# Kernel tuning notes

Hardware: AMD Instinct MI355X
Metric: run time of the kernel (lower is better)

## Reference

```python
import jax, jax.numpy as jnp
import numpy as np

BATCH, T, H, N = 16, 4096, 512, 512  # batch, seq_len, d_model, d_hidden
R_MAX, R_MIN, MAX_PHASE = 1.0, 0.0, 6.28


def setup_inputs() -> dict:
    key = jax.random.key(0)
    ks = jax.random.split(key, 8)
    u_k = jax.random.normal(ks[0], (BATCH, T, H), jnp.float32)
    x0_real = jnp.zeros((BATCH, N), jnp.float32)
    x0_imag = jnp.zeros((BATCH, N), jnp.float32)
    # LRU eigenvalue parameterization (Orvieto et al. 2023)
    u1 = jax.random.uniform(ks[1], (N,), jnp.float32)
    u2 = jax.random.uniform(ks[2], (N,), jnp.float32)
    nu_log = jnp.log(-0.5 * jnp.log(u1 * (R_MAX**2 - R_MIN**2) + R_MIN**2))
    theta_log = jnp.log(MAX_PHASE * u2)
    B_re = jax.random.normal(ks[3], (N, H), jnp.float32) / np.sqrt(2.0 * H)
    B_im = jax.random.normal(ks[4], (N, H), jnp.float32) / np.sqrt(2.0 * H)
    C_re = jax.random.normal(ks[5], (H, N), jnp.float32) / np.sqrt(N)
    C_im = jax.random.normal(ks[6], (H, N), jnp.float32) / np.sqrt(N)
    D = jax.random.normal(ks[7], (H,), jnp.float32)
    return dict(x0_real=x0_real, x0_imag=x0_imag, u_k=u_k, nu_log=nu_log,
                theta_log=theta_log, B_re=B_re, B_im=B_im, C_re=C_re,
                C_im=C_im, D=D)


def reference(x0_real, x0_imag, u_k, nu_log, theta_log, B_re, B_im, C_re, C_im, D):
    # diagonal complex eigenvalues lambda in the unit disk
    lam = jnp.exp(-jnp.exp(nu_log) + 1j * jnp.exp(theta_log))          # [N] complex64
    gamma = jnp.sqrt(1.0 - jnp.abs(lam) ** 2).astype(jnp.float32)       # [N]
    Bmat = (B_re + 1j * B_im) * gamma[:, None]                          # [N,H]
    # input projection: Bu[b,t,n] = sum_h Bmat[n,h] * u[b,t,h]
    Bu = jnp.einsum('bth,nh->btn', u_k.astype(jnp.complex64), Bmat)     # [B,T,N]
    # fold initial state into first step: x_1 = lam*x_0 + Bu_1
    x0 = x0_real + 1j * x0_imag                                         # [B,N]
    Bu = Bu.at[:, 0].add(lam[None, :] * x0)
    a = jnp.broadcast_to(lam, Bu.shape)                                 # [B,T,N]

    def combine(e1, e2):
        a1, b1 = e1
        a2, b2 = e2
        return a1 * a2, a2 * b1 + b2

    # parallel associative scan of x_k = lam*x_{k-1} + Bu_k
    _, xs = jax.lax.associative_scan(combine, (a, Bu), axis=1)          # [B,T,N]
    C = C_re + 1j * C_im                                                # [H,N]
    outs = jnp.einsum('btn,hn->bth', xs, C).real + D * u_k              # [B,T,H]
    return xs[:, -1], outs
```

## Files before the change

kernel.cpp:

```cpp
#include <hip/hip_runtime.h>

#define BATCH 16
#define TSEQ  4096
#define HDIM  512
#define NDIM  512
#define NCHUNK 64
#define LCHUNK 64

using f32x4  = __attribute__((ext_vector_type(4))) float;
using bf16x8 = __attribute__((ext_vector_type(8))) short;

typedef const __attribute__((address_space(1))) void GV;
typedef __attribute__((address_space(3))) void LV;

__device__ __forceinline__ void gload16(const void* g, void* l) {
  __builtin_amdgcn_global_load_lds((GV*)g, (LV*)l, 16, 0, 0);
}
__device__ __forceinline__ unsigned short f2bf(float f) {
  unsigned u = __float_as_uint(f);
  return (unsigned short)((u + 0x7fffu + ((u >> 16) & 1u)) >> 16);
}
__device__ __forceinline__ float bf2f(unsigned short s) {
  return __uint_as_float(((unsigned)s) << 16);
}

__global__ void prep_params(const float* __restrict__ nu_log,
                            const float* __restrict__ theta_log,
                            float* lam_re, float* lam_im, float* gam,
                            float* lamL_re, float* lamL_im) {
  int n = threadIdx.x;
  float en = expf(nu_log[n]);
  float th = expf(theta_log[n]);
  float r  = expf(-en);
  lam_re[n] = r * cosf(th);
  lam_im[n] = r * sinf(th);
  float r2 = expf(-2.f * en);
  gam[n] = sqrtf(fmaxf(1.f - r2, 0.f));
  float rL  = expf(-(float)LCHUNK * en);
  float thL = (float)LCHUNK * th;
  lamL_re[n] = rL * cosf(thL);
  lamL_im[n] = rL * sinf(thL);
}

__global__ void prep_bcat(const float* __restrict__ B_re, const float* __restrict__ B_im,
                          const float* __restrict__ gam, unsigned short* __restrict__ Bcat) {
  int idx = blockIdx.x * 256 + threadIdx.x;
  int h   = idx & (HDIM - 1);
  int row = idx >> 9;
  int n   = row >> 1;
  float g = gam[n];
  float v = (row & 1) ? B_im[n * HDIM + h] : B_re[n * HDIM + h];
  Bcat[idx] = f2bf(g * v);
}

__global__ void prep_ccat(const float* __restrict__ C_re, const float* __restrict__ C_im,
                          unsigned short* __restrict__ Ccat) {
  int idx = blockIdx.x * 256 + threadIdx.x;
  int col = idx & (2 * NDIM - 1);
  int h   = idx >> 10;
  int n   = col >> 1;
  float v = (col & 1) ? -C_im[h * NDIM + n] : C_re[h * NDIM + n];
  Ccat[idx] = f2bf(v);
}

__global__ void conv_u(const float4* __restrict__ u, ushort4* __restrict__ ub, int n4) {
  int idx = blockIdx.x * 256 + threadIdx.x;
  if (idx >= n4) return;
  float4 v = u[idx];
  ushort4 o;
  o.x = f2bf(v.x); o.y = f2bf(v.y); o.z = f2bf(v.z); o.w = f2bf(v.w);
  ub[idx] = o;
}

template <int K, bool OUTBF>
__global__ __launch_bounds__(256, 3)
void gemm97(const unsigned short* __restrict__ A,
            const unsigned short* __restrict__ Bm,
            void* __restrict__ Co, int Ncol, int Nd,
            const unsigned short* __restrict__ ub,
            const float* __restrict__ Dv) {
  __shared__ char lds[32768];
  const int tid  = threadIdx.x;
  const int wave = tid >> 6, lane = tid & 63;
  const int wr = (wave >> 1) * 64, wc = (wave & 1) * 64;

  int nwg = gridDim.x;
  int bid = blockIdx.x;
  int wg  = (bid & 7) * (nwg >> 3) + (bid >> 3);
  int bn = wg % Ncol, bm = wg / Ncol;
  const long rowBase = (long)bm * 128;
  const long colBase = (long)bn * 128;

  const int colE = 8 * ((tid & 7) ^ ((tid >> 3) & 7));
  const unsigned short* srcA[4];
  const unsigned short* srcB[4];
#pragma unroll
  for (int r = 0; r < 4; r++) {
    srcA[r] = A  + (rowBase + r * 32 + (tid >> 3)) * (long)K + colE;
    srcB[r] = Bm + (colBase + r * 32 + (tid >> 3)) * (long)K + colE;
  }

  f32x4 acc[4][4];
#pragma unroll
  for (int i = 0; i < 4; i++)
#pragma unroll
    for (int j = 0; j < 4; j++) acc[i][j] = (f32x4){0.f, 0.f, 0.f, 0.f};

  const int rsub = lane & 15;
  const int sx   = (lane & 7) << 4;
  const int ke   = (lane >> 4) << 4;

  for (int kt = 0; kt < K; kt += 64) {
    __syncthreads();
#pragma unroll
    for (int r = 0; r < 4; r++) {
      gload16(srcA[r] + kt, &lds[r * 4096 + tid * 16]);
      gload16(srcB[r] + kt, &lds[16384 + r * 4096 + tid * 16]);
    }
    __syncthreads();
#pragma unroll
    for (int kk = 0; kk < 64; kk += 32) {
      bf16x8 af[4], bf[4];
#pragma unroll
      for (int i = 0; i < 4; i++) {
        int off = (((wr + i * 16 + rsub) << 7) + kk * 2 + ke) ^ sx;
        af[i] = *(const bf16x8*)&lds[off];
      }
#pragma unroll
      for (int j = 0; j < 4; j++) {
        int off = 16384 + ((((wc + j * 16 + rsub) << 7) + kk * 2 + ke) ^ sx);
        bf[j] = *(const bf16x8*)&lds[off];
      }
#pragma unroll
      for (int i = 0; i < 4; i++)
#pragma unroll
        for (int j = 0; j < 4; j++)
          acc[i][j] = __builtin_amdgcn_mfma_f32_16x16x32_bf16(af[i], bf[j], acc[i][j], 0, 0, 0);
    }
  }

  const int cc = lane & 15, r4 = (lane >> 4) * 4;
#pragma unroll
  for (int i = 0; i < 4; i++) {
#pragma unroll
    for (int j = 0; j < 4; j++) {
      long col = colBase + wc + j * 16 + cc;
#pragma unroll
      for (int r = 0; r < 4; r++) {
        long row = rowBase + wr + i * 16 + r4 + r;
        if (OUTBF) {
          ((unsigned short*)Co)[row * (long)Nd + col] = f2bf(acc[i][j][r]);
        } else {
          float d = Dv[col];
          ((float*)Co)[row * (long)Nd + col] =
              acc[i][j][r] + d * bf2f(ub[row * (long)Nd + col]);
        }
      }
    }
  }
}

__global__ void scan_carry(const unsigned* __restrict__ Bu,
                           const float* __restrict__ lam_re, const float* __restrict__ lam_im,
                           float2* __restrict__ V) {
  int idx  = blockIdx.x * 256 + threadIdx.x;
  int n    = idx & (NDIM - 1);
  int c    = (idx >> 9) & (NCHUNK - 1);
  int bloc = idx >> 15;
  float lr = lam_re[n], li = lam_im[n];
  float xr = 0.f, xi = 0.f;
  long base = ((long)bloc * TSEQ + c * LCHUNK) * NDIM + n;
#pragma unroll 4
  for (int j = 0; j < LCHUNK; j++) {
    unsigned pv = Bu[base + (long)j * NDIM];
    float br = bf2f((unsigned short)(pv & 0xffff));
    float bi = bf2f((unsigned short)(pv >> 16));
    float nr = lr * xr - li * xi + br;
    float ni = lr * xi + li * xr + bi;
    xr = nr; xi = ni;
  }
  V[idx] = make_float2(xr, xi);
}

__global__ void scan_combine(const float2* __restrict__ V,
                             const float* __restrict__ lamL_re, const float* __restrict__ lamL_im,
                             const float* __restrict__ x0r, const float* __restrict__ x0i,
                             int b0, float2* __restrict__ In) {
  int idx  = blockIdx.x * 256 + threadIdx.x;
  int n    = idx & (NDIM - 1);
  int bloc = idx >> 9;
  int b    = b0 + bloc;
  float lr = lamL_re[n], li = lamL_im[n];
  float sr = x0r[b * NDIM + n], si = x0i[b * NDIM + n];
  long base = (long)bloc * NCHUNK * NDIM + n;
  for (int c = 0; c < NCHUNK; c++) {
    In[base + c * NDIM] = make_float2(sr, si);
    float2 v = V[base + c * NDIM];
    float nr = lr * sr - li * si + v.x;
    float ni = lr * si + li * sr + v.y;
    sr = nr; si = ni;
  }
}

__global__ void scan_apply(const unsigned* __restrict__ Bu, const float2* __restrict__ In,
                           const float* __restrict__ lam_re, const float* __restrict__ lam_im,
                           unsigned int* __restrict__ xsb, float* __restrict__ fs,
                           int b0, int fs_mode) {
  int idx  = blockIdx.x * 256 + threadIdx.x;
  int n    = idx & (NDIM - 1);
  int c    = (idx >> 9) & (NCHUNK - 1);
  int bloc = idx >> 15;
  float lr = lam_re[n], li = lam_im[n];
  float2 s = In[idx];
  float xr = s.x, xi = s.y;
  long base = ((long)bloc * TSEQ + c * LCHUNK) * NDIM + n;
#pragma unroll 4
  for (int j = 0; j < LCHUNK; j++) {
    unsigned pv = Bu[base + (long)j * NDIM];
    float br = bf2f((unsigned short)(pv & 0xffff));
    float bi = bf2f((unsigned short)(pv >> 16));
    float nr = lr * xr - li * xi + br;
    float ni = lr * xi + li * xr + bi;
    xr = nr; xi = ni;
    xsb[base + (long)j * NDIM] = (unsigned)f2bf(xr) | ((unsigned)f2bf(xi) << 16);
  }
  if (c == NCHUNK - 1 && fs_mode >= 0) {
    int b = b0 + bloc;
    if (fs_mode == 1) {
      fs[(size_t)(b * NDIM + n) * 2]     = xr;
      fs[(size_t)(b * NDIM + n) * 2 + 1] = xi;
    } else {
      fs[(size_t)(b * NDIM + n)] = xr;
    }
  }
}

extern "C" void kernel_launch(void* const* d_in, const int* in_sizes, int n_in,
                              void* d_out, int out_size, void* d_ws, size_t ws_size,
                              hipStream_t stream) {
  const float* x0r       = (const float*)d_in[0];
  const float* x0i       = (const float*)d_in[1];
  const float* u         = (const float*)d_in[2];
  const float* nu_log    = (const float*)d_in[3];
  const float* theta_log = (const float*)d_in[4];
  const float* B_re      = (const float*)d_in[5];
  const float* B_im      = (const float*)d_in[6];
  const float* C_re      = (const float*)d_in[7];
  const float* C_im      = (const float*)d_in[8];
  const float* Dv        = (const float*)d_in[9];

  char* ws = (char*)d_ws;
  size_t off = 0;
  auto alloc = [&](size_t bytes) {
    char* p = ws + off;
    off = (off + bytes + 255) & ~(size_t)255;
    return p;
  };

  float* lam_re  = (float*)alloc(NDIM * 4);
  float* lam_im  = (float*)alloc(NDIM * 4);
  float* gam     = (float*)alloc(NDIM * 4);
  float* lamL_re = (float*)alloc(NDIM * 4);
  float* lamL_im = (float*)alloc(NDIM * 4);
  unsigned short* Bcat = (unsigned short*)alloc((size_t)2 * NDIM * HDIM * 2);
  unsigned short* Ccat = (unsigned short*)alloc((size_t)HDIM * 2 * NDIM * 2);

  const size_t per_batch =
      (size_t)TSEQ * HDIM * 2 +
      (size_t)TSEQ * NDIM * 4 +
      (size_t)TSEQ * NDIM * 4 +
      (size_t)2 * NCHUNK * NDIM * 8 +
      4096;
  int G = 16;
  while (G > 1 && off + (size_t)G * per_batch > ws_size) G >>= 1;

  ushort4*      ub  = (ushort4*)alloc((size_t)G * TSEQ * HDIM * 2);
  unsigned*     Bu  = (unsigned*)alloc((size_t)G * TSEQ * NDIM * 4);
  unsigned int* xsb = (unsigned int*)alloc((size_t)G * TSEQ * NDIM * 4);
  float2*       V   = (float2*)alloc((size_t)G * NCHUNK * NDIM * 8);
  float2*       In  = (float2*)alloc((size_t)G * NCHUNK * NDIM * 8);

  const long outs_elems = (long)BATCH * TSEQ * HDIM;
  long out0 = (long)out_size - outs_elems;
  int fs_mode;
  if (out0 >= 16384)     fs_mode = 1;
  else if (out0 >= 8192) fs_mode = 0;
  else { out0 = 0;       fs_mode = -1; }

  float* fs   = (float*)d_out;
  float* outs = (float*)d_out + out0;

  prep_params<<<1, NDIM, 0, stream>>>(nu_log, theta_log, lam_re, lam_im, gam, lamL_re, lamL_im);
  prep_bcat<<<(2 * NDIM * HDIM) / 256, 256, 0, stream>>>(B_re, B_im, gam, Bcat);
  prep_ccat<<<(HDIM * 2 * NDIM) / 256, 256, 0, stream>>>(C_re, C_im, Ccat);

  for (int b0 = 0; b0 < BATCH; b0 += G) {
    const float* ug = u + (size_t)b0 * TSEQ * HDIM;
    int Mloc = G * TSEQ;
    int n4 = Mloc * HDIM / 4;
    conv_u<<<(n4 + 255) / 256, 256, 0, stream>>>((const float4*)ug, ub, n4);

    int nwg1 = (Mloc / 128) * 8;
    gemm97<512, true><<<nwg1, 256, 0, stream>>>(
        (const unsigned short*)ub, Bcat, Bu, 8, 2 * NDIM, nullptr, nullptr);

    scan_carry<<<(G * NCHUNK * NDIM) / 256, 256, 0, stream>>>(Bu, lam_re, lam_im, V);
    scan_combine<<<(G * NDIM) / 256, 256, 0, stream>>>(
        V, lamL_re, lamL_im, x0r, x0i, b0, In);
    scan_apply<<<(G * NCHUNK * NDIM) / 256, 256, 0, stream>>>(
        Bu, In, lam_re, lam_im, xsb, fs, b0, fs_mode);

    int nwg2 = (Mloc / 128) * 4;
    gemm97<1024, false><<<nwg2, 256, 0, stream>>>(
        (const unsigned short*)xsb, Ccat, outs + (size_t)b0 * TSEQ * HDIM,
        4, HDIM, (const unsigned short*)ub, Dv);
  }
}
```

Before: 317.4 us.

## Replace 4-wave 128x128 GEMM tiles with single-wave 64x64 workgroups

Both projection GEMMs are restructured so that each workgroup is one wavefront computing a 64x64 tile, replacing four waves sharing a 128x128 tile. The __syncthreads barriers give way to a per-wave vmcnt wait, and LDS per block is halved. The aim is to remove block-level synchronisation and allow more concurrent workgroups. In exchange, each wave now reloads A and B tiles that were previously shared across four waves, which raises global and LDS traffic per FLOP. The loads still have no double buffering, and the single LDS buffer is overwritten each k-step without a barrier after the MFMA reads, so correctness relies on in-order execution within the wave.

```diff
diff --git a/kernel.cpp b/kernel.cpp
--- a/kernel.cpp
+++ b/kernel.cpp
@@ -73,32 +73,25 @@
 }
 
 template <int K, bool OUTBF>
-__global__ __launch_bounds__(256, 3)
-void gemm97(const unsigned short* __restrict__ A,
-            const unsigned short* __restrict__ Bm,
-            void* __restrict__ Co, int Ncol, int Nd,
-            const unsigned short* __restrict__ ub,
-            const float* __restrict__ Dv) {
-  __shared__ char lds[32768];
-  const int tid  = threadIdx.x;
-  const int wave = tid >> 6, lane = tid & 63;
-  const int wr = (wave >> 1) * 64, wc = (wave & 1) * 64;
+__global__ __launch_bounds__(64, 3)
+void gemmw(const unsigned short* __restrict__ A,
+           const unsigned short* __restrict__ Bm,
+           void* __restrict__ Co, int Ncol, int Nd,
+           const unsigned short* __restrict__ ub,
+           const float* __restrict__ Dv) {
+  __shared__ char lds[16384];
+  const int lane = threadIdx.x;
 
   int nwg = gridDim.x;
   int bid = blockIdx.x;
   int wg  = (bid & 7) * (nwg >> 3) + (bid >> 3);
   int bn = wg % Ncol, bm = wg / Ncol;
-  const long rowBase = (long)bm * 128;
-  const long colBase = (long)bn * 128;
-
-  const int colE = 8 * ((tid & 7) ^ ((tid >> 3) & 7));
-  const unsigned short* srcA[4];
-  const unsigned short* srcB[4];
-#pragma unroll
-  for (int r = 0; r < 4; r++) {
-    srcA[r] = A  + (rowBase + r * 32 + (tid >> 3)) * (long)K + colE;
-    srcB[r] = Bm + (colBase + r * 32 + (tid >> 3)) * (long)K + colE;
-  }
+  const long rowBase = (long)bm * 64;
+  const long colBase = (long)bn * 64;
+
+  const int colE = 8 * ((lane & 7) ^ (lane >> 3));
+  const unsigned short* srcA = A  + (rowBase + (lane >> 3)) * (long)K + colE;
+  const unsigned short* srcB = Bm + (colBase + (lane >> 3)) * (long)K + colE;
 
   f32x4 acc[4][4];
 #pragma unroll
@@ -111,24 +104,24 @@
   const int ke   = (lane >> 4) << 4;
 
   for (int kt = 0; kt < K; kt += 64) {
-    __syncthreads();
-#pragma unroll
-    for (int r = 0; r < 4; r++) {
-      gload16(srcA[r] + kt, &lds[r * 4096 + tid * 16]);
-      gload16(srcB[r] + kt, &lds[16384 + r * 4096 + tid * 16]);
-    }
-    __syncthreads();
-#pragma unroll
-    for (int kk = 0; kk < 64; kk += 32) {
+#pragma unroll
+    for (int r = 0; r < 8; r++)
+      gload16(srcA + kt + (long)r * 8 * K, &lds[r * 1024 + lane * 16]);
+#pragma unroll
+    for (int r = 0; r < 8; r++)
+      gload16(srcB + kt + (long)r * 8 * K, &lds[8192 + r * 1024 + lane * 16]);
+    asm volatile("s_waitcnt vmcnt(0)" ::: "memory");
+#pragma unroll
+    for (int kk2 = 0; kk2 < 2; kk2++) {
       bf16x8 af[4], bf[4];
 #pragma unroll
       for (int i = 0; i < 4; i++) {
-        int off = (((wr + i * 16 + rsub) << 7) + kk * 2 + ke) ^ sx;
+        int off = (((i * 16 + rsub) << 7) + kk2 * 64 + ke) ^ sx;
         af[i] = *(const bf16x8*)&lds[off];
       }
 #pragma unroll
       for (int j = 0; j < 4; j++) {
-        int off = 16384 + ((((wc + j * 16 + rsub) << 7) + kk * 2 + ke) ^ sx);
+        int off = 8192 + ((((j * 16 + rsub) << 7) + kk2 * 64 + ke) ^ sx);
         bf[j] = *(const bf16x8*)&lds[off];
       }
 #pragma unroll
@@ -144,10 +137,10 @@
   for (int i = 0; i < 4; i++) {
 #pragma unroll
     for (int j = 0; j < 4; j++) {
-      long col = colBase + wc + j * 16 + cc;
+      long col = colBase + j * 16 + cc;
 #pragma unroll
       for (int r = 0; r < 4; r++) {
-        long row = rowBase + wr + i * 16 + r4 + r;
+        long row = rowBase + i * 16 + r4 + r;
         if (OUTBF) {
           ((unsigned short*)Co)[row * (long)Nd + col] = f2bf(acc[i][j][r]);
         } else {
@@ -300,9 +293,9 @@
     int n4 = Mloc * HDIM / 4;
     conv_u<<<(n4 + 255) / 256, 256, 0, stream>>>((const float4*)ug, ub, n4);
 
-    int nwg1 = (Mloc / 128) * 8;
-    gemm97<512, true><<<nwg1, 256, 0, stream>>>(
-        (const unsigned short*)ub, Bcat, Bu, 8, 2 * NDIM, nullptr, nullptr);
+    int nwg1 = (Mloc / 64) * 16;
+    gemmw<512, true><<<nwg1, 64, 0, stream>>>(
+        (const unsigned short*)ub, Bcat, Bu, 16, 2 * NDIM, nullptr, nullptr);
 
     scan_carry<<<(G * NCHUNK * NDIM) / 256, 256, 0, stream>>>(Bu, lam_re, lam_im, V);
     scan_combine<<<(G * NDIM) / 256, 256, 0, stream>>>(
@@ -310,9 +303,9 @@
     scan_apply<<<(G * NCHUNK * NDIM) / 256, 256, 0, stream>>>(
         Bu, In, lam_re, lam_im, xsb, fs, b0, fs_mode);
 
-    int nwg2 = (Mloc / 128) * 4;
-    gemm97<1024, false><<<nwg2, 256, 0, stream>>>(
+    int nwg2 = (Mloc / 64) * 8;
+    gemmw<1024, false><<<nwg2, 64, 0, stream>>>(
         (const unsigned short*)xsb, Ccat, outs + (size_t)b0 * TSEQ * HDIM,
-        4, HDIM, (const unsigned short*)ub, Dv);
-  }
-}
+        8, HDIM, (const unsigned short*)ub, Dv);
+  }
+}
```

Result: slower. 371.9 us (+17.2%).
